# Optimization experiments

Hardware: AMD Instinct MI355X
Metric: run time of the kernel (lower is better)

The kernel has to match this reference:

```python
import jax, jax.numpy as jnp
import numpy as np

D_STATE = 16
DT_RANK = 48
D_CONV = 4
EPS = 1e-5


def rmsnorm(x, w):
    return x * jax.lax.rsqrt(jnp.mean(x * x, axis=-1, keepdims=True) + EPS) * w


def causal_dw_conv(u, w, b):
    # u: [B,T,D], w: [D,K] depthwise causal kernel, b: [D]
    B, T, D = u.shape
    K = w.shape[1]
    up = jnp.pad(u, ((0, 0), (K - 1, 0), (0, 0)))
    acc = jnp.zeros_like(u)
    for k in range(K):  # K=4, tiny fixed loop
        acc = acc + up[:, k:k + T, :] * w[:, k]
    return acc + b


def mamba_mixer(h, ipw, cw, cb, xpw, dpw, dpb, alog, dpar, opw):
    # h: [B,T,d_model]
    B, T, _ = h.shape
    xz = h @ ipw.T                       # [B,T,2*d_inner]
    u, z = jnp.split(xz, 2, axis=-1)     # each [B,T,d_inner]
    u = jax.nn.silu(causal_dw_conv(u, cw, cb))
    xp = u @ xpw.T                       # [B,T,dt_rank+2*d_state]
    dt = xp[..., :DT_RANK]
    Bm = xp[..., DT_RANK:DT_RANK + D_STATE]
    Cm = xp[..., DT_RANK + D_STATE:]
    delta = jax.nn.softplus(dt @ dpw.T + dpb)      # [B,T,d_inner]
    A = -jnp.exp(alog)                              # [d_inner, d_state], negative
    dA = jnp.exp(delta[..., None] * A)              # [B,T,d_inner,d_state] in (0,1)
    dBu = (delta * u)[..., None] * Bm[:, :, None, :]
    # time-major for scan
    dA_t = jnp.moveaxis(dA, 1, 0)
    dBu_t = jnp.moveaxis(dBu, 1, 0)
    C_t = jnp.moveaxis(Cm, 1, 0)

    def step(hst, inp):
        a, bu, c = inp
        hst = a * hst + bu                          # [B,d_inner,d_state]
        y = jnp.einsum('bdn,bn->bd', hst, c)
        return hst, y

    h0 = jnp.zeros((B, u.shape[-1], D_STATE), u.dtype)
    _, ys = jax.lax.scan(step, h0, (dA_t, dBu_t, C_t))
    y = jnp.moveaxis(ys, 0, 1) + u * dpar           # skip via D
    y = y * jax.nn.silu(z)                          # gate
    return y @ opw.T                                # [B,T,d_model]


def setup_inputs() -> dict:
    key = jax.random.key(0)
    ks = jax.random.split(key, 16)
    L, d_model, d_inner = 4, 768, 1536
    B, C, T = 4, 256, 512
    s = 0.02
    return {
        'x': jax.random.normal(ks[0], (B, C, T), jnp.float32),
        'in_proj_w': jax.random.normal(ks[1], (L, 2 * d_inner, d_model), jnp.float32) * s,
        'conv_w': jax.random.normal(ks[2], (L, d_inner, D_CONV), jnp.float32) * 0.3,
        'conv_b': jnp.zeros((L, d_inner), jnp.float32),
        'x_proj_w': jax.random.normal(ks[3], (L, DT_RANK + 2 * D_STATE, d_inner), jnp.float32) * s,
        'dt_proj_w': jax.random.normal(ks[4], (L, d_inner, DT_RANK), jnp.float32) * 0.1,
        'dt_proj_b': jax.random.normal(ks[5], (L, d_inner), jnp.float32) * 0.1 - 4.0,
        'A_log': jax.random.uniform(ks[6], (L, d_inner, D_STATE), jnp.float32, 0.0, 1.5),
        'D_param': jax.random.uniform(ks[7], (L, d_inner), jnp.float32),
        'out_proj_w': jax.random.normal(ks[8], (L, d_model, d_inner), jnp.float32) * s,
        'norm_w': jnp.ones((L, d_model), jnp.float32),
        'norm_f_w': jnp.ones((d_model,), jnp.float32),
        'inp_w': jax.random.normal(ks[9], (d_model, C), jnp.float32) * s,
        'inp_b': jnp.zeros((d_model,), jnp.float32),
        'cls_w': jax.random.normal(ks[10], (10, d_model), jnp.float32) * s,
        'cls_b': jnp.zeros((10,), jnp.float32),
    }


def reference(x, in_proj_w, conv_w, conv_b, x_proj_w, dt_proj_w, dt_proj_b,
              A_log, D_param, out_proj_w, norm_w, norm_f_w,
              inp_w, inp_b, cls_w, cls_b):
    # x: (B, C, T) -> (B, T, C)
    xt = jnp.transpose(x, (0, 2, 1))
    h = xt @ inp_w.T + inp_b                # [B,T,d_model]
    hidden = h
    residual = None
    L = in_proj_w.shape[0]
    for l in range(L):
        residual = hidden if residual is None else hidden + residual
        normed = rmsnorm(residual, norm_w[l])
        hidden = mamba_mixer(normed, in_proj_w[l], conv_w[l], conv_b[l],
                             x_proj_w[l], dt_proj_w[l], dt_proj_b[l],
                             A_log[l], D_param[l], out_proj_w[l])
    residual = hidden + residual
    hidden = rmsnorm(residual, norm_f_w)
    pooled = hidden.mean(axis=1)            # [B,d_model]
    logits = pooled @ cls_w.T + cls_b       # [B,num_labels]
    return logits
```

## Files before the change

kernel.cpp:

```cpp
#include <hip/hip_runtime.h>
#include <math.h>

#define D_MODEL 768
#define D_INNER 1536
#define B_SZ 4
#define T_SZ 512
#define ROWS (B_SZ*T_SZ)
#define XP_N 80
#define CH 16
#define CT 32
#define XS 8
#define XKC (D_INNER/XS)
#define OS 4
#define OKC (D_INNER/OS)
#define MN_OUT (ROWS*768)

typedef __attribute__((ext_vector_type(8))) short bf16x8;
typedef __attribute__((ext_vector_type(4))) float f32x4;

#define GLL(g, l) __builtin_amdgcn_global_load_lds( \
    (const __attribute__((address_space(1))) void*)(g), \
    (__attribute__((address_space(3))) void*)(l), 16, 0, 0)

__device__ __forceinline__ float sigmoidf_(float x){ return 1.0f/(1.0f+__expf(-x)); }
__device__ __forceinline__ float siluf_(float x){ return x*sigmoidf_(x); }
__device__ __forceinline__ unsigned short f2bf(float f){
  unsigned u = __builtin_bit_cast(unsigned, f);
  u = (u + 0x7FFFu + ((u >> 16) & 1u)) >> 16;
  return (unsigned short)u;
}

__global__ void transpose_x(const float* __restrict__ x, float* __restrict__ xt){
  __shared__ float s[32][33];
  int b = blockIdx.z;
  int t0 = blockIdx.x*32, c0 = blockIdx.y*32;
  int tx = threadIdx.x, ty = threadIdx.y;
  s[ty][tx] = x[((size_t)b*256 + (c0+ty))*512 + (t0+tx)];
  __syncthreads();
  xt[((size_t)b*512 + (t0+ty))*256 + (c0+tx)] = s[tx][ty];
}

__global__ __launch_bounds__(256) void gemm_bf16(
    const unsigned short* __restrict__ A, const unsigned short* __restrict__ Wb,
    float* __restrict__ C, int M, int N, int K)
{
  __shared__ unsigned short As[128*32];
  __shared__ unsigned short Ws[128*32];
  const int tid = threadIdx.x;
  const int bm = blockIdx.y*128, bn = blockIdx.x*128;
  const int wave = tid >> 6, lane = tid & 63;
  const int wm = (wave >> 1)*64, wn = (wave & 1)*64;
  const int fr = lane & 15, quad = lane >> 4;
  f32x4 acc[4][4] = {};
  const int row0 = (wave*64 + lane) >> 2;
  const int khp  = lane & 3;
  const int khl  = (khp + 4 - ((row0 >> 1) & 3)) & 3;
  const unsigned short* Ag = A  + (size_t)(bm + row0)*K + khl*8;
  const unsigned short* Wg = Wb + (size_t)(bn + row0)*K + khl*8;
  const size_t rstep = (size_t)64*K;
  unsigned short* ldsA = As + wave*512;
  unsigned short* ldsW = Ws + wave*512;

  for (int k0 = 0; k0 < K; k0 += 32){
    GLL(Ag + k0,          ldsA);
    GLL(Ag + rstep + k0,  ldsA + 2048);
    GLL(Wg + k0,          ldsW);
    GLL(Wg + rstep + k0,  ldsW + 2048);
    __syncthreads();
    bf16x8 a[4], b[4];
    #pragma unroll
    for (int i=0;i<4;i++){
      const int row = wm + i*16 + fr;
      a[i] = *(const bf16x8*)(As + row*32 + (((quad + (row>>1)) & 3)*8));
    }
    #pragma unroll
    for (int j=0;j<4;j++){
      const int row = wn + j*16 + fr;
      b[j] = *(const bf16x8*)(Ws + row*32 + (((quad + (row>>1)) & 3)*8));
    }
    #pragma unroll
    for (int i=0;i<4;i++)
      #pragma unroll
      for (int j=0;j<4;j++)
        acc[i][j] = __builtin_amdgcn_mfma_f32_16x16x32_bf16(a[i], b[j], acc[i][j], 0, 0, 0);
    __syncthreads();
  }
  #pragma unroll
  for (int i=0;i<4;i++){
    #pragma unroll
    for (int r=0;r<4;r++){
      const int row = bm + wm + i*16 + quad*4 + r;
      float* Cp = C + (size_t)row*N + bn + wn + fr;
      #pragma unroll
      for (int j=0;j<4;j++)
        Cp[j*16] = acc[i][j][r];
    }
  }
}

__global__ __launch_bounds__(256) void gemm_bf16_sk(
    const unsigned short* __restrict__ A, const unsigned short* __restrict__ Wb,
    float* __restrict__ P0, float* __restrict__ P1, int M, int N, int K)
{
  __shared__ unsigned short As[128*32];
  __shared__ unsigned short Ws[128*32];
  const int tid = threadIdx.x;
  const int bm = blockIdx.y*128, bn = blockIdx.x*128;
  const int s = blockIdx.z;
  const int koff = s*OKC;
  const int wave = tid >> 6, lane = tid & 63;
  const int wm = (wave >> 1)*64, wn = (wave & 1)*64;
  const int fr = lane & 15, quad = lane >> 4;
  f32x4 acc[4][4] = {};
  const int row0 = (wave*64 + lane) >> 2;
  const int khp  = lane & 3;
  const int khl  = (khp + 4 - ((row0 >> 1) & 3)) & 3;
  const unsigned short* Ag = A  + (size_t)(bm + row0)*K + koff + khl*8;
  const unsigned short* Wg = Wb + (size_t)(bn + row0)*K + koff + khl*8;
  const size_t rstep = (size_t)64*K;
  unsigned short* ldsA = As + wave*512;
  unsigned short* ldsW = Ws + wave*512;

  for (int k0 = 0; k0 < OKC; k0 += 32){
    GLL(Ag + k0,          ldsA);
    GLL(Ag + rstep + k0,  ldsA + 2048);
    GLL(Wg + k0,          ldsW);
    GLL(Wg + rstep + k0,  ldsW + 2048);
    __syncthreads();
    bf16x8 a[4], b[4];
    #pragma unroll
    for (int i=0;i<4;i++){
      const int row = wm + i*16 + fr;
      a[i] = *(const bf16x8*)(As + row*32 + (((quad + (row>>1)) & 3)*8));
    }
    #pragma unroll
    for (int j=0;j<4;j++){
      const int row = wn + j*16 + fr;
      b[j] = *(const bf16x8*)(Ws + row*32 + (((quad + (row>>1)) & 3)*8));
    }
    #pragma unroll
    for (int i=0;i<4;i++)
      #pragma unroll
      for (int j=0;j<4;j++)
        acc[i][j] = __builtin_amdgcn_mfma_f32_16x16x32_bf16(a[i], b[j], acc[i][j], 0, 0, 0);
    __syncthreads();
  }
  float* Cb = (s < 2 ? P0 : P1) + (size_t)(s & 1)*MN_OUT;
  #pragma unroll
  for (int i=0;i<4;i++){
    #pragma unroll
    for (int r=0;r<4;r++){
      const int row = bm + wm + i*16 + quad*4 + r;
      float* Cp = Cb + (size_t)row*N + bn + wn + fr;
      #pragma unroll
      for (int j=0;j<4;j++)
        Cp[j*16] = acc[i][j][r];
    }
  }
}

__global__ __launch_bounds__(256) void sgemm_tn(
    const float* __restrict__ A, int lda,
    const float* __restrict__ W,
    const float* __restrict__ bias,
    float* __restrict__ C, int M, int N, int K, int act)
{
  __shared__ float As[16][64];
  __shared__ float Wsh[16][64];
  const int bm = blockIdx.y*64, bn = blockIdx.x*64;
  const int tid = threadIdx.x;
  const int tx = tid & 15, ty = tid >> 4;
  const int lm = tid & 63, lk = (tid >> 6) << 2;
  float acc[4][4] = {};
  const float* Ap = A + (size_t)(bm+lm)*lda + lk;
  const float* Wp = W + (size_t)(bn+lm)*K + lk;
  const bool wok = (bn+lm) < N;
  for (int k0 = 0; k0 < K; k0 += 16){
    float4 av = *(const float4*)(Ap + k0);
    float4 wv = wok ? *(const float4*)(Wp + k0) : make_float4(0.f,0.f,0.f,0.f);
    As[lk+0][lm]=av.x; As[lk+1][lm]=av.y; As[lk+2][lm]=av.z; As[lk+3][lm]=av.w;
    Wsh[lk+0][lm]=wv.x; Wsh[lk+1][lm]=wv.y; Wsh[lk+2][lm]=wv.z; Wsh[lk+3][lm]=wv.w;
    __syncthreads();
    #pragma unroll
    for (int k = 0; k < 16; k++){
      float a[4], w[4];
      #pragma unroll
      for (int i=0;i<4;i++) a[i] = As[k][ty*4+i];
      #pragma unroll
      for (int j=0;j<4;j++) w[j] = Wsh[k][tx*4+j];
      #pragma unroll
      for (int i=0;i<4;i++)
        #pragma unroll
        for (int j=0;j<4;j++)
          acc[i][j] += a[i]*w[j];
    }
    __syncthreads();
  }
  #pragma unroll
  for (int i=0;i<4;i++){
    const int r = bm + ty*4 + i;
    #pragma unroll
    for (int j=0;j<4;j++){
      const int n = bn + tx*4 + j;
      if (n < N){
        float v = acc[i][j] + (bias ? bias[n] : 0.f);
        if (act == 1){ v = (v > 20.f) ? v : log1pf(__expf(v)); }
        C[(size_t)r*N + n] = v;
      }
    }
  }
}

__global__ __launch_bounds__(256) void sgemm_splitk_xp(
    const float* __restrict__ A, const float* __restrict__ W,
    float* __restrict__ part)
{
  __shared__ float As[16][64];
  __shared__ float Wsh[16][64];
  const int bm = blockIdx.y*64, bn = blockIdx.x*64;
  const int s = blockIdx.z;
  const int koff = s*XKC;
  const int tid = threadIdx.x;
  const int tx = tid & 15, ty = tid >> 4;
  const int lm = tid & 63, lk = (tid >> 6) << 2;
  float acc[4][4] = {};
  const float* Ap = A + (size_t)(bm+lm)*D_INNER + koff + lk;
  const float* Wp = W + (size_t)(bn+lm)*D_INNER + koff + lk;
  const bool wok = (bn+lm) < XP_N;
  for (int k0 = 0; k0 < XKC; k0 += 16){
    float4 av = *(const float4*)(Ap + k0);
    float4 wv = wok ? *(const float4*)(Wp + k0) : make_float4(0.f,0.f,0.f,0.f);
    As[lk+0][lm]=av.x; As[lk+1][lm]=av.y; As[lk+2][lm]=av.z; As[lk+3][lm]=av.w;
    Wsh[lk+0][lm]=wv.x; Wsh[lk+1][lm]=wv.y; Wsh[lk+2][lm]=wv.z; Wsh[lk+3][lm]=wv.w;
    __syncthreads();
    #pragma unroll
    for (int k = 0; k < 16; k++){
      float a[4], w[4];
      #pragma unroll
      for (int i=0;i<4;i++) a[i] = As[k][ty*4+i];
      #pragma unroll
      for (int j=0;j<4;j++) w[j] = Wsh[k][tx*4+j];
      #pragma unroll
      for (int i=0;i<4;i++)
        #pragma unroll
        for (int j=0;j<4;j++)
          acc[i][j] += a[i]*w[j];
    }
    __syncthreads();
  }
  #pragma unroll
  for (int i=0;i<4;i++){
    const int r = bm + ty*4 + i;
    #pragma unroll
    for (int j=0;j<4;j++){
      const int n = bn + tx*4 + j;
      if (n < XP_N)
        part[((size_t)s*ROWS + r)*XP_N + n] = acc[i][j];
    }
  }
}

__global__ __launch_bounds__(256) void reduce_xp(const float* __restrict__ part,
                                                 float* __restrict__ xp){
  const int i = blockIdx.x*256 + threadIdx.x;
  if (i >= ROWS*XP_N) return;
  float s = 0.f;
  #pragma unroll
  for (int c=0;c<XS;c++) s += part[(size_t)c*ROWS*XP_N + i];
  xp[i] = s;
}

__global__ __launch_bounds__(256) void fused_norm_cast(
    float* __restrict__ resid, const float* __restrict__ P0, const float* __restrict__ P1,
    const float* __restrict__ w, unsigned short* __restrict__ obf, float* __restrict__ ofp,
    const float* __restrict__ cin1, unsigned short* __restrict__ co1, int cn1, int cnb1,
    const float* __restrict__ cin2, unsigned short* __restrict__ co2, int cn2)
{
  const int blk = blockIdx.x;
  if (blk >= 2048){
    const int cb = blk - 2048;
    const float* in; unsigned short* o; int i4;
    if (cb < cnb1){ in = cin1; o = co1; i4 = (cb*256 + threadIdx.x)*4; if (i4 >= cn1) return; }
    else { in = cin2; o = co2; i4 = ((cb-cnb1)*256 + threadIdx.x)*4; if (i4 >= cn2) return; }
    float4 v = *(const float4*)(in + i4);
    ushort4 r;
    r.x = f2bf(v.x); r.y = f2bf(v.y); r.z = f2bf(v.z); r.w = f2bf(v.w);
    *(ushort4*)(o + i4) = r;
    return;
  }
  const int row = blk;
  const int tid = threadIdx.x;
  float v[3];
  float ss = 0.f;
  #pragma unroll
  for (int i=0;i<3;i++){
    const int c = tid + i*256;
    const size_t idx = (size_t)row*768 + c;
    float r = resid[idx];
    if (P0) r += (P0[idx] + P0[MN_OUT + idx]) + (P1[idx] + P1[MN_OUT + idx]);
    v[i] = r;
    ss += r*r;
  }
  #pragma unroll
  for (int off=32; off>=1; off>>=1) ss += __shfl_xor(ss, off);
  __shared__ float sred[4];
  const int lane = tid & 63, wv = tid >> 6;
  if (lane == 0) sred[wv] = ss;
  __syncthreads();
  const float tot = sred[0]+sred[1]+sred[2]+sred[3];
  const float scale = rsqrtf(tot*(1.0f/768.0f) + 1e-5f);
  #pragma unroll
  for (int i=0;i<3;i++){
    const int c = tid + i*256;
    const size_t idx = (size_t)row*768 + c;
    if (P0) resid[idx] = v[i];
    const float o = v[i]*scale*w[c];
    if (obf) obf[idx] = f2bf(o);
    else     ofp[idx] = o;
  }
}

__global__ __launch_bounds__(256) void conv_silu(
    const float* __restrict__ xz, const float* __restrict__ cw,
    const float* __restrict__ cb, float* __restrict__ uo)
{
  const int idx = blockIdx.x*256 + threadIdx.x;
  if (idx >= ROWS*D_INNER) return;
  const int d = idx % D_INNER;
  const int row = idx / D_INNER;
  const int t = row & (T_SZ-1);
  float acc = cb[d];
  #pragma unroll
  for (int k=0;k<4;k++){
    const int tt = t - 3 + k;
    if (tt >= 0)
      acc += xz[(size_t)(row - 3 + k)*3072 + d] * cw[d*4 + k];
  }
  uo[idx] = siluf_(acc);
}

__global__ __launch_bounds__(256) void scan_pass1(
    const float* __restrict__ delta, const float* __restrict__ u,
    const float* __restrict__ xp, const float* __restrict__ alog,
    float* __restrict__ Pend, float* __restrict__ Hend)
{
  const int d = blockIdx.x*256 + threadIdx.x;
  const int b = blockIdx.y, c = blockIdx.z;
  float4 t0 = *(const float4*)(alog + d*16 + 0);
  float4 t1 = *(const float4*)(alog + d*16 + 4);
  float4 t2 = *(const float4*)(alog + d*16 + 8);
  float4 t3 = *(const float4*)(alog + d*16 + 12);
  float Av[16] = {t0.x,t0.y,t0.z,t0.w,t1.x,t1.y,t1.z,t1.w,
                  t2.x,t2.y,t2.z,t2.w,t3.x,t3.y,t3.z,t3.w};
  float h[16], P[16];
  #pragma unroll
  for (int n=0;n<16;n++){ Av[n] = -__expf(Av[n]); h[n]=0.f; P[n]=1.f; }
  const size_t row0 = (size_t)b*T_SZ + (size_t)c*CT;
  const float* dp = delta + row0*D_INNER + d;
  const float* up = u     + row0*D_INNER + d;
  const float* bp = xp    + row0*XP_N + 48;
  for (int t=0;t<CT;t++){
    const float dv = dp[(size_t)t*D_INNER];
    const float uv = up[(size_t)t*D_INNER];
    const float4 B0 = *(const float4*)(bp + (size_t)t*XP_N);
    const float4 B1 = *(const float4*)(bp + (size_t)t*XP_N + 4);
    const float4 B2 = *(const float4*)(bp + (size_t)t*XP_N + 8);
    const float4 B3 = *(const float4*)(bp + (size_t)t*XP_N + 12);
    const float Bv[16] = {B0.x,B0.y,B0.z,B0.w,B1.x,B1.y,B1.z,B1.w,
                          B2.x,B2.y,B2.z,B2.w,B3.x,B3.y,B3.z,B3.w};
    const float du = dv*uv;
    #pragma unroll
    for (int n=0;n<16;n++){
      const float dA = __expf(dv*Av[n]);
      P[n] *= dA;
      h[n] = dA*h[n] + du*Bv[n];
    }
  }
  float* Pp = Pend + ((size_t)(b*CH+c)*D_INNER + d)*16;
  float* Hp = Hend + ((size_t)(b*CH+c)*D_INNER + d)*16;
  *(float4*)(Pp+ 0) = make_float4(P[0],P[1],P[2],P[3]);
  *(float4*)(Pp+ 4) = make_float4(P[4],P[5],P[6],P[7]);
  *(float4*)(Pp+ 8) = make_float4(P[8],P[9],P[10],P[11]);
  *(float4*)(Pp+12) = make_float4(P[12],P[13],P[14],P[15]);
  *(float4*)(Hp+ 0) = make_float4(h[0],h[1],h[2],h[3]);
  *(float4*)(Hp+ 4) = make_float4(h[4],h[5],h[6],h[7]);
  *(float4*)(Hp+ 8) = make_float4(h[8],h[9],h[10],h[11]);
  *(float4*)(Hp+12) = make_float4(h[12],h[13],h[14],h[15]);
}

__global__ __launch_bounds__(256) void scan_combine(
    const float* __restrict__ Pend, const float* __restrict__ Hend,
    float* __restrict__ Hin)
{
  const int gid = blockIdx.x*256 + threadIdx.x;
  const int b = gid / (D_INNER*16);
  const int r = gid % (D_INNER*16);
  const size_t base = (size_t)b*CH*D_INNER*16 + r;
  const size_t step = (size_t)D_INNER*16;
  float h = 0.f;
  Hin[base] = 0.f;
  for (int c=0; c<CH-1; c++){
    h = Pend[base + (size_t)c*step]*h + Hend[base + (size_t)c*step];
    Hin[base + (size_t)(c+1)*step] = h;
  }
}

__global__ __launch_bounds__(256) void scan_pass3(
    const float* __restrict__ delta, const float* __restrict__ u,
    const float* __restrict__ xp, const float* __restrict__ xz,
    const float* __restrict__ alog, const float* __restrict__ Dp,
    const float* __restrict__ Hin, unsigned short* __restrict__ yb)
{
  const int d = blockIdx.x*256 + threadIdx.x;
  const int b = blockIdx.y, c = blockIdx.z;
  float4 t0 = *(const float4*)(alog + d*16 + 0);
  float4 t1 = *(const float4*)(alog + d*16 + 4);
  float4 t2 = *(const float4*)(alog + d*16 + 8);
  float4 t3 = *(const float4*)(alog + d*16 + 12);
  float Av[16] = {t0.x,t0.y,t0.z,t0.w,t1.x,t1.y,t1.z,t1.w,
                  t2.x,t2.y,t2.z,t2.w,t3.x,t3.y,t3.z,t3.w};
  #pragma unroll
  for (int n=0;n<16;n++) Av[n] = -__expf(Av[n]);
  const float* Hp = Hin + ((size_t)(b*CH+c)*D_INNER + d)*16;
  float4 h0 = *(const float4*)(Hp+0);
  float4 h1 = *(const float4*)(Hp+4);
  float4 h2 = *(const float4*)(Hp+8);
  float4 h3 = *(const float4*)(Hp+12);
  float h[16] = {h0.x,h0.y,h0.z,h0.w,h1.x,h1.y,h1.z,h1.w,
                 h2.x,h2.y,h2.z,h2.w,h3.x,h3.y,h3.z,h3.w};
  const float Dv = Dp[d];
  const size_t row0 = (size_t)b*T_SZ + (size_t)c*CT;
  const float* dp = delta + row0*D_INNER + d;
  const float* up = u     + row0*D_INNER + d;
  const float* bp = xp    + row0*XP_N + 48;
  const float* cp = xp    + row0*XP_N + 64;
  const float* zp = xz    + row0*3072 + 1536 + d;
  unsigned short* yp = yb + row0*D_INNER + d;
  for (int t=0;t<CT;t++){
    const float dv = dp[(size_t)t*D_INNER];
    const float uv = up[(size_t)t*D_INNER];
    const float zv = zp[(size_t)t*3072];
    const float4 B0 = *(const float4*)(bp + (size_t)t*XP_N);
    const float4 B1 = *(const float4*)(bp + (size_t)t*XP_N + 4);
    const float4 B2 = *(const float4*)(bp + (size_t)t*XP_N + 8);
    const float4 B3 = *(const float4*)(bp + (size_t)t*XP_N + 12);
    const float4 C0 = *(const float4*)(cp + (size_t)t*XP_N);
    const float4 C1 = *(const float4*)(cp + (size_t)t*XP_N + 4);
    const float4 C2 = *(const float4*)(cp + (size_t)t*XP_N + 8);
    const float4 C3 = *(const float4*)(cp + (size_t)t*XP_N + 12);
    const float Bv[16] = {B0.x,B0.y,B0.z,B0.w,B1.x,B1.y,B1.z,B1.w,
                          B2.x,B2.y,B2.z,B2.w,B3.x,B3.y,B3.z,B3.w};
    const float Cv[16] = {C0.x,C0.y,C0.z,C0.w,C1.x,C1.y,C1.z,C1.w,
                          C2.x,C2.y,C2.z,C2.w,C3.x,C3.y,C3.z,C3.w};
    const float du = dv*uv;
    float p = 0.f;
    #pragma unroll
    for (int n=0;n<16;n++){
      const float dA = __expf(dv*Av[n]);
      h[n] = dA*h[n] + du*Bv[n];
      p += h[n]*Cv[n];
    }
    yp[(size_t)t*D_INNER] = f2bf((p + uv*Dv)*siluf_(zv));
  }
}

__global__ __launch_bounds__(256) void pool_partial(const float* __restrict__ normed,
                                                    float* __restrict__ part){
  const int i = blockIdx.x*256 + threadIdx.x;
  const int s = blockIdx.y;
  const int b = i / 768, m = i % 768;
  float sum = 0.f;
  const float* p = normed + ((size_t)b*T_SZ + s*32)*768 + m;
  #pragma unroll
  for (int t=0; t<32; t++) sum += p[(size_t)t*768];
  part[s*3072 + i] = sum;
}

__global__ __launch_bounds__(256) void pool_cls(const float* __restrict__ part,
                                                const float* __restrict__ cw,
                                                const float* __restrict__ cb,
                                                float* __restrict__ out){
  __shared__ float ls[768];
  const int b = blockIdx.x;
  const int tid = threadIdx.x;
  #pragma unroll
  for (int i=0;i<3;i++){
    const int m = tid + i*256;
    float s = 0.f;
    #pragma unroll
    for (int c=0;c<16;c++) s += part[c*3072 + b*768 + m];
    ls[m] = s * (1.0f/T_SZ);
  }
  __syncthreads();
  const int wave = tid >> 6, lane = tid & 63;
  for (int o = wave; o < 10; o += 4){
    float s = 0.f;
    for (int k = lane; k < 768; k += 64) s += ls[k]*cw[o*768 + k];
    #pragma unroll
    for (int off=32; off>=1; off>>=1) s += __shfl_xor(s, off);
    if (lane == 0) out[b*10 + o] = s + cb[o];
  }
}

extern "C" void kernel_launch(void* const* d_in, const int* in_sizes, int n_in,
                              void* d_out, int out_size, void* d_ws, size_t ws_size,
                              hipStream_t stream) {
  const float* x         = (const float*)d_in[0];
  const float* in_proj_w = (const float*)d_in[1];
  const float* conv_w    = (const float*)d_in[2];
  const float* conv_b    = (const float*)d_in[3];
  const float* x_proj_w  = (const float*)d_in[4];
  const float* dt_proj_w = (const float*)d_in[5];
  const float* dt_proj_b = (const float*)d_in[6];
  const float* A_log     = (const float*)d_in[7];
  const float* D_param   = (const float*)d_in[8];
  const float* out_proj_w= (const float*)d_in[9];
  const float* norm_w    = (const float*)d_in[10];
  const float* norm_f_w  = (const float*)d_in[11];
  const float* inp_w     = (const float*)d_in[12];
  const float* inp_b     = (const float*)d_in[13];
  const float* cls_w     = (const float*)d_in[14];
  const float* cls_b     = (const float*)d_in[15];
  float* out = (float*)d_out;

  char* ws = (char*)d_ws;
  auto carve = [&](size_t nelem)->float* {
    float* p = (float*)ws;
    ws += ((nelem*sizeof(float) + 255)/256)*256;
    return p;
  };
  float* xt     = carve((size_t)ROWS*256);
  float* resid  = carve((size_t)ROWS*768);
  float* normed = carve((size_t)ROWS*768);
  float* hidden = carve((size_t)ROWS*768);
  float* xz     = carve((size_t)ROWS*3072);
  float* ucv    = carve((size_t)ROWS*1536);
  float* xp     = carve((size_t)ROWS*XP_N);
  float* delta  = carve((size_t)ROWS*1536);
  float* ybf_f  = carve((size_t)ROWS*1536/2);
  float* wbi_f  = carve((size_t)(3072*768)/2);
  float* wbo_f  = carve((size_t)(768*1536)/2);
  float* Hin    = carve((size_t)B_SZ*CH*D_INNER*16);
  float* xpart  = carve((size_t)XS*ROWS*XP_N);
  float* ppool  = carve((size_t)16*3072);
  float* pooled = carve((size_t)B_SZ*768);
  (void)pooled;

  unsigned short* normedb = (unsigned short*)normed;
  unsigned short* ybf = (unsigned short*)ybf_f;
  unsigned short* wbi = (unsigned short*)wbi_f;
  unsigned short* wbo = (unsigned short*)wbo_f;
  float* Pend = normed;
  float* Hend = hidden;

  transpose_x<<<dim3(16,8,4), dim3(32,32), 0, stream>>>(x, xt);
  sgemm_tn<<<dim3(12,32), 256, 0, stream>>>(xt, 256, inp_w, inp_b, resid, ROWS, 768, 256, 0);

  for (int l = 0; l < 4; l++){
    fused_norm_cast<<<2048 + 2304 + 1152, 256, 0, stream>>>(
        resid, l ? delta : nullptr, l ? ucv : nullptr,
        norm_w + (size_t)l*768, normedb, nullptr,
        in_proj_w + (size_t)l*3072*768, wbi, 3072*768, 2304,
        out_proj_w + (size_t)l*768*1536, wbo, 768*1536);
    gemm_bf16<<<dim3(24,16), 256, 0, stream>>>(normedb, wbi, xz, ROWS, 3072, 768);
    conv_silu<<<(ROWS*D_INNER)/256, 256, 0, stream>>>(xz, conv_w + (size_t)l*1536*4, conv_b + (size_t)l*1536, ucv);
    sgemm_splitk_xp<<<dim3(2,32,XS), 256, 0, stream>>>(ucv, x_proj_w + (size_t)l*XP_N*1536, xpart);
    reduce_xp<<<(ROWS*XP_N)/256, 256, 0, stream>>>(xpart, xp);
    sgemm_tn<<<dim3(24,32), 256, 0, stream>>>(xp, XP_N, dt_proj_w + (size_t)l*1536*48, dt_proj_b + (size_t)l*1536,
                                              delta, ROWS, 1536, 48, 1);
    scan_pass1<<<dim3(6,B_SZ,CH-1), 256, 0, stream>>>(delta, ucv, xp,
                                               A_log + (size_t)l*1536*16, Pend, Hend);
    scan_combine<<<(B_SZ*D_INNER*16)/256, 256, 0, stream>>>(Pend, Hend, Hin);
    scan_pass3<<<dim3(6,B_SZ,CH), 256, 0, stream>>>(delta, ucv, xp, xz,
                                               A_log + (size_t)l*1536*16, D_param + (size_t)l*1536, Hin, ybf);
    gemm_bf16_sk<<<dim3(6,16,OS), 256, 0, stream>>>(ybf, wbo, delta, ucv, ROWS, 768, 1536);
  }

  fused_norm_cast<<<2048, 256, 0, stream>>>(
      resid, delta, ucv, norm_f_w, nullptr, normed,
      nullptr, nullptr, 0, 0, nullptr, nullptr, 0);
  pool_partial<<<dim3(12,16), 256, 0, stream>>>(normed, ppool);
  pool_cls<<<4, 256, 0, stream>>>(ppool, cls_w, cls_b, out);
}
```

Baseline: 826.6 us.

## Move remaining fp32 GEMMs to bf16 MFMA and batch all weight casts upfront

Result: no change. 830.8 us (+0.5%).

```diff
diff --git a/kernel.cpp b/kernel.cpp
--- a/kernel.cpp
+++ b/kernel.cpp
@@ -29,19 +29,61 @@
   u = (u + 0x7FFFu + ((u >> 16) & 1u)) >> 16;
   return (unsigned short)u;
 }
-
-__global__ void transpose_x(const float* __restrict__ x, float* __restrict__ xt){
+__device__ __forceinline__ ushort4 cvt4(float4 v){
+  ushort4 r; r.x=f2bf(v.x); r.y=f2bf(v.y); r.z=f2bf(v.z); r.w=f2bf(v.w); return r;
+}
+
+#define CA_N0 9437184LL
+#define CA_N1 4718592LL
+#define CA_N2 196608LL
+#define CA_N3 786432LL
+#define CA_N4 393216LL
+__global__ __launch_bounds__(256) void cast_all(
+    const float* __restrict__ ipw, unsigned short* __restrict__ wbi,
+    const float* __restrict__ opw, unsigned short* __restrict__ wbo,
+    const float* __restrict__ inpw, unsigned short* __restrict__ inpwb,
+    const float* __restrict__ xpw, unsigned short* __restrict__ xpwb,
+    const float* __restrict__ dtw, unsigned short* __restrict__ dtwb)
+{
+  long long i4 = ((long long)blockIdx.x*256 + threadIdx.x)*4;
+  if (i4 < CA_N0){ *(ushort4*)(wbi + i4) = cvt4(*(const float4*)(ipw + i4)); return; }
+  i4 -= CA_N0;
+  if (i4 < CA_N1){ *(ushort4*)(wbo + i4) = cvt4(*(const float4*)(opw + i4)); return; }
+  i4 -= CA_N1;
+  if (i4 < CA_N2){ *(ushort4*)(inpwb + i4) = cvt4(*(const float4*)(inpw + i4)); return; }
+  i4 -= CA_N2;
+  if (i4 < CA_N3){
+    const long long l = i4 / (128*1536), rem = i4 % (128*1536);
+    const long long r = rem / 1536, k = rem % 1536;
+    ushort4 o;
+    if (r < 80) o = cvt4(*(const float4*)(xpw + (l*80 + r)*1536 + k));
+    else { o.x=0;o.y=0;o.z=0;o.w=0; }
+    *(ushort4*)(xpwb + i4) = o; return;
+  }
+  i4 -= CA_N3;
+  if (i4 < CA_N4){
+    const long long l = i4 / (1536*64), rem = i4 % (1536*64);
+    const long long r = rem / 64, c = rem % 64;
+    ushort4 o;
+    if (c < 48) o = cvt4(*(const float4*)(dtw + (l*1536 + r)*48 + c));
+    else { o.x=0;o.y=0;o.z=0;o.w=0; }
+    *(ushort4*)(dtwb + i4) = o;
+  }
+}
+
+__global__ void transpose_x(const float* __restrict__ x, unsigned short* __restrict__ xtb){
   __shared__ float s[32][33];
   int b = blockIdx.z;
   int t0 = blockIdx.x*32, c0 = blockIdx.y*32;
   int tx = threadIdx.x, ty = threadIdx.y;
   s[ty][tx] = x[((size_t)b*256 + (c0+ty))*512 + (t0+tx)];
   __syncthreads();
-  xt[((size_t)b*512 + (t0+ty))*256 + (c0+tx)] = s[tx][ty];
+  xtb[((size_t)b*512 + (t0+ty))*256 + (c0+tx)] = f2bf(s[tx][ty]);
 }
 
 __global__ __launch_bounds__(256) void gemm_bf16(
     const unsigned short* __restrict__ A, const unsigned short* __restrict__ Wb,
+    const float* __restrict__ bias,
     float* __restrict__ C, int M, int N, int K)
 {
   __shared__ unsigned short As[128*32];
@@ -92,8 +134,10 @@
       const int row = bm + wm + i*16 + quad*4 + r;
       float* Cp = C + (size_t)row*N + bn + wn + fr;
       #pragma unroll
-      for (int j=0;j<4;j++)
-        Cp[j*16] = acc[i][j][r];
+      for (int j=0;j<4;j++){
+        const int col = bn + wn + j*16 + fr;
+        Cp[j*16] = acc[i][j][r] + (bias ? bias[col] : 0.f);
+      }
     }
   }
 }
@@ -159,136 +203,149 @@
   }
 }
 
-__global__ __launch_bounds__(256) void sgemm_tn(
-    const float* __restrict__ A, int lda,
-    const float* __restrict__ W,
-    const float* __restrict__ bias,
-    float* __restrict__ C, int M, int N, int K, int act)
-{
-  __shared__ float As[16][64];
-  __shared__ float Wsh[16][64];
-  const int bm = blockIdx.y*64, bn = blockIdx.x*64;
+__global__ __launch_bounds__(256) void gemm_bf16_xp(
+    const unsigned short* __restrict__ A, const unsigned short* __restrict__ Wb,
+    float* __restrict__ part)
+{
+  __shared__ unsigned short As[128*32];
+  __shared__ unsigned short Ws[128*32];
   const int tid = threadIdx.x;
-  const int tx = tid & 15, ty = tid >> 4;
-  const int lm = tid & 63, lk = (tid >> 6) << 2;
-  float acc[4][4] = {};
-  const float* Ap = A + (size_t)(bm+lm)*lda + lk;
-  const float* Wp = W + (size_t)(bn+lm)*K + lk;
-  const bool wok = (bn+lm) < N;
-  for (int k0 = 0; k0 < K; k0 += 16){
-    float4 av = *(const float4*)(Ap + k0);
-    float4 wv = wok ? *(const float4*)(Wp + k0) : make_float4(0.f,0.f,0.f,0.f);
-    As[lk+0][lm]=av.x; As[lk+1][lm]=av.y; As[lk+2][lm]=av.z; As[lk+3][lm]=av.w;
-    Wsh[lk+0][lm]=wv.x; Wsh[lk+1][lm]=wv.y; Wsh[lk+2][lm]=wv.z; Wsh[lk+3][lm]=wv.w;
-    __syncthreads();
-    #pragma unroll
-    for (int k = 0; k < 16; k++){
-      float a[4], w[4];
-      #pragma unroll
-      for (int i=0;i<4;i++) a[i] = As[k][ty*4+i];
-      #pragma unroll
-      for (int j=0;j<4;j++) w[j] = Wsh[k][tx*4+j];
-      #pragma unroll
-      for (int i=0;i<4;i++)
-        #pragma unroll
-        for (int j=0;j<4;j++)
-          acc[i][j] += a[i]*w[j];
-    }
+  const int bm = blockIdx.x*128;
+  const int s = blockIdx.y;
+  const int koff = s*XKC;
+  const int wave = tid >> 6, lane = tid & 63;
+  const int wm = (wave >> 1)*64, wn = (wave & 1)*64;
+  const int fr = lane & 15, quad = lane >> 4;
+  f32x4 acc[4][4] = {};
+  const int row0 = (wave*64 + lane) >> 2;
+  const int khp  = lane & 3;
+  const int khl  = (khp + 4 - ((row0 >> 1) & 3)) & 3;
+  const unsigned short* Ag = A  + (size_t)(bm + row0)*D_INNER + koff + khl*8;
+  const unsigned short* Wg = Wb + (size_t)row0*D_INNER + koff + khl*8;
+  const size_t rstep = (size_t)64*D_INNER;
+  unsigned short* ldsA = As + wave*512;
+  unsigned short* ldsW = Ws + wave*512;
+
+  for (int k0 = 0; k0 < XKC; k0 += 32){
+    GLL(Ag + k0,          ldsA);
+    GLL(Ag + rstep + k0,  ldsA + 2048);
+    GLL(Wg + k0,          ldsW);
+    GLL(Wg + rstep + k0,  ldsW + 2048);
+    __syncthreads();
+    bf16x8 a[4], b[4];
+    #pragma unroll
+    for (int i=0;i<4;i++){
+      const int row = wm + i*16 + fr;
+      a[i] = *(const bf16x8*)(As + row*32 + (((quad + (row>>1)) & 3)*8));
+    }
+    #pragma unroll
+    for (int j=0;j<4;j++){
+      const int row = wn + j*16 + fr;
+      b[j] = *(const bf16x8*)(Ws + row*32 + (((quad + (row>>1)) & 3)*8));
+    }
+    #pragma unroll
+    for (int i=0;i<4;i++)
+      #pragma unroll
+      for (int j=0;j<4;j++)
+        acc[i][j] = __builtin_amdgcn_mfma_f32_16x16x32_bf16(a[i], b[j], acc[i][j], 0, 0, 0);
     __syncthreads();
   }
   #pragma unroll
   for (int i=0;i<4;i++){
-    const int r = bm + ty*4 + i;
-    #pragma unroll
-    for (int j=0;j<4;j++){
-      const int n = bn + tx*4 + j;
-      if (n < N){
-        float v = acc[i][j] + (bias ? bias[n] : 0.f);
-        if (act == 1){ v = (v > 20.f) ? v : log1pf(__expf(v)); }
-        C[(size_t)r*N + n] = v;
+    #pragma unroll
+    for (int r=0;r<4;r++){
+      const int row = bm + wm + i*16 + quad*4 + r;
+      #pragma unroll
+      for (int j=0;j<4;j++){
+        const int col = wn + j*16 + fr;
+        if (col < XP_N)
+          part[((size_t)s*ROWS + row)*XP_N + col] = acc[i][j][r];
       }
     }
   }
 }
 
-__global__ __launch_bounds__(256) void sgemm_splitk_xp(
-    const float* __restrict__ A, const float* __restrict__ W,
-    float* __restrict__ part)
-{
-  __shared__ float As[16][64];
-  __shared__ float Wsh[16][64];
-  const int bm = blockIdx.y*64, bn = blockIdx.x*64;
-  const int s = blockIdx.z;
-  const int koff = s*XKC;
-  const int tid = threadIdx.x;
-  const int tx = tid & 15, ty = tid >> 4;
-  const int lm = tid & 63, lk = (tid >> 6) << 2;
-  float acc[4][4] = {};
-  const float* Ap = A + (size_t)(bm+lm)*D_INNER + koff + lk;
-  const float* Wp = W + (size_t)(bn+lm)*D_INNER + koff + lk;
-  const bool wok = (bn+lm) < XP_N;
-  for (int k0 = 0; k0 < XKC; k0 += 16){
-    float4 av = *(const float4*)(Ap + k0);
-    float4 wv = wok ? *(const float4*)(Wp + k0) : make_float4(0.f,0.f,0.f,0.f);
-    As[lk+0][lm]=av.x; As[lk+1][lm]=av.y; As[lk+2][lm]=av.z; As[lk+3][lm]=av.w;
-    Wsh[lk+0][lm]=wv.x; Wsh[lk+1][lm]=wv.y; Wsh[lk+2][lm]=wv.z; Wsh[lk+3][lm]=wv.w;
-    __syncthreads();
-    #pragma unroll
-    for (int k = 0; k < 16; k++){
-      float a[4], w[4];
-      #pragma unroll
-      for (int i=0;i<4;i++) a[i] = As[k][ty*4+i];
-      #pragma unroll
-      for (int j=0;j<4;j++) w[j] = Wsh[k][tx*4+j];
-      #pragma unroll
-      for (int i=0;i<4;i++)
-        #pragma unroll
-        for (int j=0;j<4;j++)
-          acc[i][j] += a[i]*w[j];
-    }
-    __syncthreads();
-  }
-  #pragma unroll
-  for (int i=0;i<4;i++){
-    const int r = bm + ty*4 + i;
-    #pragma unroll
-    for (int j=0;j<4;j++){
-      const int n = bn + tx*4 + j;
-      if (n < XP_N)
-        part[((size_t)s*ROWS + r)*XP_N + n] = acc[i][j];
-    }
-  }
-}
-
 __global__ __launch_bounds__(256) void reduce_xp(const float* __restrict__ part,
-                                                 float* __restrict__ xp){
+                                                 float* __restrict__ xp,
+                                                 unsigned short* __restrict__ xpb){
   const int i = blockIdx.x*256 + threadIdx.x;
   if (i >= ROWS*XP_N) return;
+  const int row = i / XP_N, c = i % XP_N;
   float s = 0.f;
   #pragma unroll
-  for (int c=0;c<XS;c++) s += part[(size_t)c*ROWS*XP_N + i];
+  for (int k=0;k<XS;k++) s += part[(size_t)k*ROWS*XP_N + i];
   xp[i] = s;
-}
-
-__global__ __launch_bounds__(256) void fused_norm_cast(
+  if (c < 48) xpb[row*64 + c] = f2bf(s);
+  else if (c < 64) xpb[row*64 + c] = 0;
+}
+
+__global__ __launch_bounds__(256) void gemm_bf16_dt(
+    const unsigned short* __restrict__ A, const unsigned short* __restrict__ Wb,
+    const float* __restrict__ bias, float* __restrict__ C)
+{
+  __shared__ unsigned short As[128*32];
+  __shared__ unsigned short Ws[128*32];
+  const int tid = threadIdx.x;
+  const int bm = blockIdx.y*128, bn = blockIdx.x*128;
+  const int wave = tid >> 6, lane = tid & 63;
+  const int wm = (wave >> 1)*64, wn = (wave & 1)*64;
+  const int fr = lane & 15, quad = lane >> 4;
+  f32x4 acc[4][4] = {};
+  const int row0 = (wave*64 + lane) >> 2;
+  const int khp  = lane & 3;
+  const int khl  = (khp + 4 - ((row0 >> 1) & 3)) & 3;
+  const unsigned short* Ag = A  + (size_t)(bm + row0)*64 + khl*8;
+  const unsigned short* Wg = Wb + (size_t)(bn + row0)*64 + khl*8;
+  const size_t rstepA = (size_t)64*64;
+  unsigned short* ldsA = As + wave*512;
+  unsigned short* ldsW = Ws + wave*512;
+
+  for (int k0 = 0; k0 < 64; k0 += 32){
+    GLL(Ag + k0,           ldsA);
+    GLL(Ag + rstepA + k0,  ldsA + 2048);
+    GLL(Wg + k0,           ldsW);
+    GLL(Wg + rstepA + k0,  ldsW + 2048);
+    __syncthreads();
+    bf16x8 a[4], b[4];
+    #pragma unroll
+    for (int i=0;i<4;i++){
+      const int row = wm + i*16 + fr;
+      a[i] = *(const bf16x8*)(As + row*32 + (((quad + (row>>1)) & 3)*8));
+    }
+    #pragma unroll
+    for (int j=0;j<4;j++){
+      const int row = wn + j*16 + fr;
+      b[j] = *(const bf16x8*)(Ws + row*32 + (((quad + (row>>1)) & 3)*8));
+    }
+    #pragma unroll
+    for (int i=0;i<4;i++)
+      #pragma unroll
+      for (int j=0;j<4;j++)
+        acc[i][j] = __builtin_amdgcn_mfma_f32_16x16x32_bf16(a[i], b[j], acc[i][j], 0, 0, 0);
+    __syncthreads();
+  }
+  #pragma unroll
+  for (int i=0;i<4;i++){
+    #pragma unroll
+    for (int r=0;r<4;r++){
+      const int row = bm + wm + i*16 + quad*4 + r;
+      float* Cp = C + (size_t)row*D_INNER + bn + wn + fr;
+      #pragma unroll
+      for (int j=0;j<4;j++){
+        const int col = bn + wn + j*16 + fr;
+        float v = acc[i][j][r] + bias[col];
+        v = (v > 20.f) ? v : log1pf(__expf(v));
+        Cp[j*16] = v;
+      }
+    }
+  }
+}
+
+__global__ __launch_bounds__(256) void fused_norm(
     float* __restrict__ resid, const float* __restrict__ P0, const float* __restrict__ P1,
-    const float* __restrict__ w, unsigned short* __restrict__ obf, float* __restrict__ ofp,
-    const float* __restrict__ cin1, unsigned short* __restrict__ co1, int cn1, int cnb1,
-    const float* __restrict__ cin2, unsigned short* __restrict__ co2, int cn2)
-{
-  const int blk = blockIdx.x;
-  if (blk >= 2048){
-    const int cb = blk - 2048;
-    const float* in; unsigned short* o; int i4;
-    if (cb < cnb1){ in = cin1; o = co1; i4 = (cb*256 + threadIdx.x)*4; if (i4 >= cn1) return; }
-    else { in = cin2; o = co2; i4 = ((cb-cnb1)*256 + threadIdx.x)*4; if (i4 >= cn2) return; }
-    float4 v = *(const float4*)(in + i4);
-    ushort4 r;
-    r.x = f2bf(v.x); r.y = f2bf(v.y); r.z = f2bf(v.z); r.w = f2bf(v.w);
-    *(ushort4*)(o + i4) = r;
-    return;
-  }
-  const int row = blk;
+    const float* __restrict__ w, unsigned short* __restrict__ obf, float* __restrict__ ofp)
+{
+  const int row = blockIdx.x;
   const int tid = threadIdx.x;
   float v[3];
   float ss = 0.f;
@@ -322,7 +379,8 @@
 
 __global__ __launch_bounds__(256) void conv_silu(
     const float* __restrict__ xz, const float* __restrict__ cw,
-    const float* __restrict__ cb, float* __restrict__ uo)
+    const float* __restrict__ cb, float* __restrict__ uo,
+    unsigned short* __restrict__ ub)
 {
   const int idx = blockIdx.x*256 + threadIdx.x;
   if (idx >= ROWS*D_INNER) return;
@@ -336,7 +394,9 @@
     if (tt >= 0)
       acc += xz[(size_t)(row - 3 + k)*3072 + d] * cw[d*4 + k];
   }
-  uo[idx] = siluf_(acc);
+  const float s = siluf_(acc);
+  uo[idx] = s;
+  ub[idx] = f2bf(s);
 }
 
 __global__ __launch_bounds__(256) void scan_pass1(
@@ -388,28 +448,12 @@
   *(float4*)(Hp+12) = make_float4(h[12],h[13],h[14],h[15]);
 }
 
-__global__ __launch_bounds__(256) void scan_combine(
-    const float* __restrict__ Pend, const float* __restrict__ Hend,
-    float* __restrict__ Hin)
-{
-  const int gid = blockIdx.x*256 + threadIdx.x;
-  const int b = gid / (D_INNER*16);
-  const int r = gid % (D_INNER*16);
-  const size_t base = (size_t)b*CH*D_INNER*16 + r;
-  const size_t step = (size_t)D_INNER*16;
-  float h = 0.f;
-  Hin[base] = 0.f;
-  for (int c=0; c<CH-1; c++){
-    h = Pend[base + (size_t)c*step]*h + Hend[base + (size_t)c*step];
-    Hin[base + (size_t)(c+1)*step] = h;
-  }
-}
-
 __global__ __launch_bounds__(256) void scan_pass3(
     const float* __restrict__ delta, const float* __restrict__ u,
     const float* __restrict__ xp, const float* __restrict__ xz,
     const float* __restrict__ alog, const float* __restrict__ Dp,
-    const float* __restrict__ Hin, unsigned short* __restrict__ yb)
+    const float* __restrict__ Pend, const float* __restrict__ Hend,
+    unsigned short* __restrict__ yb)
 {
   const int d = blockIdx.x*256 + threadIdx.x;
   const int b = blockIdx.y, c = blockIdx.z;
@@ -419,15 +463,23 @@
   float4 t3 = *(const float4*)(alog + d*16 + 12);
   float Av[16] = {t0.x,t0.y,t0.z,t0.w,t1.x,t1.y,t1.z,t1.w,
                   t2.x,t2.y,t2.z,t2.w,t3.x,t3.y,t3.z,t3.w};
-  #pragma unroll
-  for (int n=0;n<16;n++) Av[n] = -__expf(Av[n]);
-  const float* Hp = Hin + ((size_t)(b*CH+c)*D_INNER + d)*16;
-  float4 h0 = *(const float4*)(Hp+0);
-  float4 h1 = *(const float4*)(Hp+4);
-  float4 h2 = *(const float4*)(Hp+8);
-  float4 h3 = *(const float4*)(Hp+12);
-  float h[16] = {h0.x,h0.y,h0.z,h0.w,h1.x,h1.y,h1.z,h1.w,
-                 h2.x,h2.y,h2.z,h2.w,h3.x,h3.y,h3.z,h3.w};
+  float h[16];
+  #pragma unroll
+  for (int n=0;n<16;n++){ Av[n] = -__expf(Av[n]); h[n] = 0.f; }
+  for (int cc=0; cc<c; cc++){
+    const float* Pp = Pend + ((size_t)(b*CH+cc)*D_INNER + d)*16;
+    const float* Hp = Hend + ((size_t)(b*CH+cc)*D_INNER + d)*16;
+    float4 p0 = *(const float4*)(Pp+0),  p1 = *(const float4*)(Pp+4);
+    float4 p2 = *(const float4*)(Pp+8),  p3 = *(const float4*)(Pp+12);
+    float4 q0 = *(const float4*)(Hp+0),  q1 = *(const float4*)(Hp+4);
+    float4 q2 = *(const float4*)(Hp+8),  q3 = *(const float4*)(Hp+12);
+    const float Pv[16] = {p0.x,p0.y,p0.z,p0.w,p1.x,p1.y,p1.z,p1.w,
+                          p2.x,p2.y,p2.z,p2.w,p3.x,p3.y,p3.z,p3.w};
+    const float Hv[16] = {q0.x,q0.y,q0.z,q0.w,q1.x,q1.y,q1.z,q1.w,
+                          q2.x,q2.y,q2.z,q2.w,q3.x,q3.y,q3.z,q3.w};
+    #pragma unroll
+    for (int n=0;n<16;n++) h[n] = Pv[n]*h[n] + Hv[n];
+  }
   const float Dv = Dp[d];
   const size_t row0 = (size_t)b*T_SZ + (size_t)c*CT;
   const float* dp = delta + row0*D_INNER + d;
@@ -529,7 +581,7 @@
     ws += ((nelem*sizeof(float) + 255)/256)*256;
     return p;
   };
-  float* xt     = carve((size_t)ROWS*256);
+  float* xtb_f  = carve((size_t)ROWS*256/2);
   float* resid  = carve((size_t)ROWS*768);
   float* normed = carve((size_t)ROWS*768);
   float* hidden = carve((size_t)ROWS*768);
@@ -538,47 +590,55 @@
   float* xp     = carve((size_t)ROWS*XP_N);
   float* delta  = carve((size_t)ROWS*1536);
   float* ybf_f  = carve((size_t)ROWS*1536/2);
-  float* wbi_f  = carve((size_t)(3072*768)/2);
-  float* wbo_f  = carve((size_t)(768*1536)/2);
-  float* Hin    = carve((size_t)B_SZ*CH*D_INNER*16);
+  float* ubf_f  = carve((size_t)ROWS*1536/2);
+  float* xpb_f  = carve((size_t)ROWS*64/2);
+  float* wbi_f  = carve((size_t)CA_N0/2);
+  float* wbo_f  = carve((size_t)CA_N1/2);
+  float* wip_f  = carve((size_t)CA_N2/2);
+  float* wxp_f  = carve((size_t)CA_N3/2);
+  float* wdt_f  = carve((size_t)CA_N4/2);
   float* xpart  = carve((size_t)XS*ROWS*XP_N);
   float* ppool  = carve((size_t)16*3072);
-  float* pooled = carve((size_t)B_SZ*768);
-  (void)pooled;
-
+
+  unsigned short* xtb = (unsigned short*)xtb_f;
   unsigned short* normedb = (unsigned short*)normed;
   unsigned short* ybf = (unsigned short*)ybf_f;
+  unsigned short* ubf = (unsigned short*)ubf_f;
+  unsigned short* xpb = (unsigned short*)xpb_f;
   unsigned short* wbi = (unsigned short*)wbi_f;
   unsigned short* wbo = (unsigned short*)wbo_f;
+  unsigned short* wip = (unsigned short*)wip_f;
+  unsigned short* wxp = (unsigned short*)wxp_f;
+  unsigned short* wdt = (unsigned short*)wdt_f;
   float* Pend = normed;
   float* Hend = hidden;
 
-  transpose_x<<<dim3(16,8,4), dim3(32,32), 0, stream>>>(x, xt);
-  sgemm_tn<<<dim3(12,32), 256, 0, stream>>>(xt, 256, inp_w, inp_b, resid, ROWS, 768, 256, 0);
+  cast_all<<<15168, 256, 0, stream>>>(in_proj_w, wbi, out_proj_w, wbo,
+                                      inp_w, wip, x_proj_w, wxp, dt_proj_w, wdt);
+  transpose_x<<<dim3(16,8,4), dim3(32,32), 0, stream>>>(x, xtb);
+  gemm_bf16<<<dim3(6,16), 256, 0, stream>>>(xtb, wip, inp_b, resid, ROWS, 768, 256);
 
   for (int l = 0; l < 4; l++){
-    fused_norm_cast<<<2048 + 2304 + 1152, 256, 0, stream>>>(
-        resid, l ? delta : nullptr, l ? ucv : nullptr,
-        norm_w + (size_t)l*768, normedb, nullptr,
-        in_proj_w + (size_t)l*3072*768, wbi, 3072*768, 2304,
-        out_proj_w + (size_t)l*768*1536, wbo, 768*1536);
-    gemm_bf16<<<dim3(24,16), 256, 0, stream>>>(normedb, wbi, xz, ROWS, 3072, 768);
-    conv_silu<<<(ROWS*D_INNER)/256, 256, 0, stream>>>(xz, conv_w + (size_t)l*1536*4, conv_b + (size_t)l*1536, ucv);
-    sgemm_splitk_xp<<<dim3(2,32,XS), 256, 0, stream>>>(ucv, x_proj_w + (size_t)l*XP_N*1536, xpart);
-    reduce_xp<<<(ROWS*XP_N)/256, 256, 0, stream>>>(xpart, xp);
-    sgemm_tn<<<dim3(24,32), 256, 0, stream>>>(xp, XP_N, dt_proj_w + (size_t)l*1536*48, dt_proj_b + (size_t)l*1536,
-                                              delta, ROWS, 1536, 48, 1);
+    fused_norm<<<2048, 256, 0, stream>>>(resid, l ? delta : nullptr, l ? ucv : nullptr,
+                                         norm_w + (size_t)l*768, normedb, nullptr);
+    gemm_bf16<<<dim3(24,16), 256, 0, stream>>>(normedb, wbi + (size_t)l*3072*768, nullptr,
+                                               xz, ROWS, 3072, 768);
+    conv_silu<<<(ROWS*D_INNER)/256, 256, 0, stream>>>(xz, conv_w + (size_t)l*1536*4,
+                                                      conv_b + (size_t)l*1536, ucv, ubf);
+    gemm_bf16_xp<<<dim3(16,XS), 256, 0, stream>>>(ubf, wxp + (size_t)l*128*1536, xpart);
+    reduce_xp<<<(ROWS*XP_N)/256, 256, 0, stream>>>(xpart, xp, xpb);
+    gemm_bf16_dt<<<dim3(12,16), 256, 0, stream>>>(xpb, wdt + (size_t)l*1536*64,
+                                                  dt_proj_b + (size_t)l*1536, delta);
     scan_pass1<<<dim3(6,B_SZ,CH-1), 256, 0, stream>>>(delta, ucv, xp,
                                                A_log + (size_t)l*1536*16, Pend, Hend);
-    scan_combine<<<(B_SZ*D_INNER*16)/256, 256, 0, stream>>>(Pend, Hend, Hin);
     scan_pass3<<<dim3(6,B_SZ,CH), 256, 0, stream>>>(delta, ucv, xp, xz,
-                                               A_log + (size_t)l*1536*16, D_param + (size_t)l*1536, Hin, ybf);
-    gemm_bf16_sk<<<dim3(6,16,OS), 256, 0, stream>>>(ybf, wbo, delta, ucv, ROWS, 768, 1536);
-  }
-
-  fused_norm_cast<<<2048, 256, 0, stream>>>(
-      resid, delta, ucv, norm_f_w, nullptr, normed,
-      nullptr, nullptr, 0, 0, nullptr, nullptr, 0);
+                                               A_log + (size_t)l*1536*16, D_param + (size_t)l*1536,
+                                               Pend, Hend, ybf);
+    gemm_bf16_sk<<<dim3(6,16,OS), 256, 0, stream>>>(ybf, wbo + (size_t)l*768*1536,
+                                                    delta, ucv, ROWS, 768, 1536);
+  }
+
+  fused_norm<<<2048, 256, 0, stream>>>(resid, delta, ucv, norm_f_w, nullptr, normed);
   pool_partial<<<dim3(12,16), 256, 0, stream>>>(normed, ppool);
   pool_cls<<<4, 256, 0, stream>>>(ppool, cls_w, cls_b, out);
 }
```
